# Performance work log

Measured on AMD Instinct MI355X. Metric: run time of the kernel, lower is better.

Reference implementation:

```python
import jax, jax.numpy as jnp
import numpy as np

N = 1_000_000   # total nodes
B = 1024        # number of graphs
H = 64          # node feature dim / LSTM hidden
STEPS = 5       # Set2Set processing steps
PROJ = 128      # projection_dim


def setup_inputs() -> dict:
    key = jax.random.key(0)
    ks = jax.random.split(key, 12)
    x = jax.random.normal(ks[0], (N, H), dtype=jnp.float32)
    batch = jnp.sort(jax.random.randint(ks[1], (N,), 0, B)).astype(jnp.int64)
    s = 1.0 / np.sqrt(H)
    # torch.nn.LSTM(input_size=2H, hidden_size=H), gate order i,f,g,o
    W_ih = jax.random.uniform(ks[2], (4 * H, 2 * H), minval=-s, maxval=s, dtype=jnp.float32)
    W_hh = jax.random.uniform(ks[3], (4 * H, H), minval=-s, maxval=s, dtype=jnp.float32)
    b_ih = jax.random.uniform(ks[4], (4 * H,), minval=-s, maxval=s, dtype=jnp.float32)
    b_hh = jax.random.uniform(ks[5], (4 * H,), minval=-s, maxval=s, dtype=jnp.float32)
    s1 = 1.0 / np.sqrt(2 * H)
    W1 = jax.random.uniform(ks[6], (256, 2 * H), minval=-s1, maxval=s1, dtype=jnp.float32)
    b1 = jax.random.uniform(ks[7], (256,), minval=-s1, maxval=s1, dtype=jnp.float32)
    s2 = 1.0 / np.sqrt(256)
    W2 = jax.random.uniform(ks[8], (PROJ, 256), minval=-s2, maxval=s2, dtype=jnp.float32)
    b2 = jax.random.uniform(ks[9], (PROJ,), minval=-s2, maxval=s2, dtype=jnp.float32)
    return {"x": x, "batch": batch, "W_ih": W_ih, "W_hh": W_hh, "b_ih": b_ih,
            "b_hh": b_hh, "W1": W1, "b1": b1, "W2": W2, "b2": b2}


def _set2set(x, batch, W_ih, W_hh, b_ih, b_hh):
    q_star = jnp.zeros((B, 2 * H), x.dtype)
    h = jnp.zeros((B, H), x.dtype)
    c = jnp.zeros((B, H), x.dtype)
    for _ in range(STEPS):
        gates = q_star @ W_ih.T + b_ih + h @ W_hh.T + b_hh
        i, f, g, o = jnp.split(gates, 4, axis=-1)
        i = jax.nn.sigmoid(i); f = jax.nn.sigmoid(f)
        g = jnp.tanh(g); o = jax.nn.sigmoid(o)
        c = f * c + i * g
        h = o * jnp.tanh(c)
        q = h  # [B, H]
        # segment-wise attention over ragged node sets
        e = jnp.sum(x * q[batch], axis=-1)                         # [N]
        emax = jax.ops.segment_max(e, batch, num_segments=B)       # [B]
        a = jnp.exp(e - emax[batch])
        denom = jax.ops.segment_sum(a, batch, num_segments=B)
        a = a / jnp.maximum(denom, 1e-16)[batch]
        r = jax.ops.segment_sum(a[:, None] * x, batch, num_segments=B)  # [B, H]
        q_star = jnp.concatenate([q, r], axis=-1)
    return q_star


def reference(x, batch, W_ih, W_hh, b_ih, b_hh, W1, b1, W2, b2):
    out = _set2set(x, batch, W_ih, W_hh, b_ih, b_hh)   # [B, 2H]
    out = out @ W1.T + b1                               # [B, 256]
    out = jax.nn.relu(out) @ W2.T + b2                  # [B, PROJ]
    return out
```

## Files before the change

### kernel.cpp

```cpp
#include <hip/hip_runtime.h>
#include <float.h>
#include <math.h>

#define NB 1024
#define HD 64
#define NSTEPS 5
#define SPLIT 4

__device__ __forceinline__ float sigmoidf_(float x) {
    return 1.0f / (1.0f + __expf(-x));
}

__global__ void seg_bounds_kernel(const int* __restrict__ batch,
                                  int* __restrict__ seg_start, int n) {
    int i = blockIdx.x * blockDim.x + threadIdx.x;
    if (i >= n) return;
    int b = batch[i];
    if (i == 0) {
        for (int j = 0; j <= b; ++j) seg_start[j] = 0;
    } else {
        int pb = batch[i - 1];
        for (int j = pb + 1; j <= b; ++j) seg_start[j] = i;
    }
    if (i == n - 1) {
        for (int j = b + 1; j <= NB; ++j) seg_start[j] = n;
    }
}

__global__ void lstm_kernel(const float* __restrict__ W_ih,
                            const float* __restrict__ W_hh,
                            const float* __restrict__ b_ih,
                            const float* __restrict__ b_hh,
                            const float* __restrict__ pm,
                            const float* __restrict__ ps,
                            const float* __restrict__ pr,
                            float* __restrict__ h,
                            float* __restrict__ c,
                            int first) {
    const int G = 8;
    int g0 = blockIdx.x * G;
    __shared__ float s_qs[G][128];
    __shared__ float s_gates[G][256];
    int tid = threadIdx.x;

    if (!first) {
        for (int idx = tid; idx < G * 64; idx += 256) {
            int g = idx >> 6, k = idx & 63;
            s_qs[g][k] = h[(g0 + g) * 64 + k];
        }
        for (int idx = tid; idx < G * 64; idx += 256) {
            int g = idx >> 6, k = idx & 63;
            int b = g0 + g;
            float m0 = pm[b * SPLIT + 0], m1 = pm[b * SPLIT + 1];
            float m2 = pm[b * SPLIT + 2], m3 = pm[b * SPLIT + 3];
            float M = fmaxf(fmaxf(m0, m1), fmaxf(m2, m3));
            float w0 = __expf(m0 - M), w1 = __expf(m1 - M);
            float w2 = __expf(m2 - M), w3 = __expf(m3 - M);
            float S = ps[b * SPLIT + 0] * w0 + ps[b * SPLIT + 1] * w1
                    + ps[b * SPLIT + 2] * w2 + ps[b * SPLIT + 3] * w3;
            float rf = pr[(b * SPLIT + 0) * 64 + k] * w0
                     + pr[(b * SPLIT + 1) * 64 + k] * w1
                     + pr[(b * SPLIT + 2) * 64 + k] * w2
                     + pr[(b * SPLIT + 3) * 64 + k] * w3;
            s_qs[g][64 + k] = rf / fmaxf(S, 1e-16f);
        }
        __syncthreads();
    }

    int j = tid;
    float acc[G];
    float bias = b_ih[j] + b_hh[j];
#pragma unroll
    for (int g = 0; g < G; ++g) acc[g] = bias;

    if (!first) {
        const float4* wih = (const float4*)(W_ih + j * 128);
#pragma unroll 4
        for (int k4 = 0; k4 < 32; ++k4) {
            float4 w = wih[k4];
#pragma unroll
            for (int g = 0; g < G; ++g) {
                acc[g] = fmaf(w.x, s_qs[g][k4 * 4 + 0], acc[g]);
                acc[g] = fmaf(w.y, s_qs[g][k4 * 4 + 1], acc[g]);
                acc[g] = fmaf(w.z, s_qs[g][k4 * 4 + 2], acc[g]);
                acc[g] = fmaf(w.w, s_qs[g][k4 * 4 + 3], acc[g]);
            }
        }
        const float4* whh = (const float4*)(W_hh + j * 64);
#pragma unroll 4
        for (int k4 = 0; k4 < 16; ++k4) {
            float4 w = whh[k4];
#pragma unroll
            for (int g = 0; g < G; ++g) {
                acc[g] = fmaf(w.x, s_qs[g][k4 * 4 + 0], acc[g]);
                acc[g] = fmaf(w.y, s_qs[g][k4 * 4 + 1], acc[g]);
                acc[g] = fmaf(w.z, s_qs[g][k4 * 4 + 2], acc[g]);
                acc[g] = fmaf(w.w, s_qs[g][k4 * 4 + 3], acc[g]);
            }
        }
    }
#pragma unroll
    for (int g = 0; g < G; ++g) s_gates[g][j] = acc[g];
    __syncthreads();

    for (int idx = tid; idx < G * 64; idx += 256) {
        int g = idx >> 6, jj = idx & 63;
        int gb = g0 + g;
        float ig = sigmoidf_(s_gates[g][jj]);
        float fg = sigmoidf_(s_gates[g][jj + 64]);
        float gg = tanhf(s_gates[g][jj + 128]);
        float og = sigmoidf_(s_gates[g][jj + 192]);
        float cprev = first ? 0.0f : c[gb * 64 + jj];
        float cn = fmaf(fg, cprev, ig * gg);
        float hn = og * tanhf(cn);
        c[gb * 64 + jj] = cn;
        h[gb * 64 + jj] = hn;
    }
}

__global__ __launch_bounds__(256) void attn_kernel(const float* __restrict__ x,
                                                   const int* __restrict__ seg_start,
                                                   const float* __restrict__ h,
                                                   float* __restrict__ pm,
                                                   float* __restrict__ ps,
                                                   float* __restrict__ pr) {
    int bs = blockIdx.x;
    int b = bs >> 2;
    int slice = bs & (SPLIT - 1);
    int s0 = seg_start[b], e0 = seg_start[b + 1];
    int len = e0 - s0;
    int s = s0 + (int)(((long long)len * slice) >> 2);
    int e = s0 + (int)(((long long)len * (slice + 1)) >> 2);

    int tid = threadIdx.x;
    int lane = tid & 63;
    int wave = tid >> 6;
    int quad = lane >> 2;
    int p = lane & 3;

    float q[16];
    const float* qsrc = h + b * 64 + p * 16;
#pragma unroll
    for (int k = 0; k < 16; ++k) q[k] = qsrc[k];

    float m = -FLT_MAX, sum = 0.0f;
    float r[16];
#pragma unroll
    for (int k = 0; k < 16; ++k) r[k] = 0.0f;

    for (int base = s; base < e; base += 64) {
        int node = base + wave * 16 + quad;
        bool valid = node < e;
        int nc = valid ? node : (e - 1);
        const float4* xp = (const float4*)(x + (size_t)nc * 64 + p * 16);
        float4 a0 = xp[0], a1 = xp[1], a2 = xp[2], a3 = xp[3];
        float xv[16];
        xv[0] = a0.x; xv[1] = a0.y; xv[2] = a0.z; xv[3] = a0.w;
        xv[4] = a1.x; xv[5] = a1.y; xv[6] = a1.z; xv[7] = a1.w;
        xv[8] = a2.x; xv[9] = a2.y; xv[10] = a2.z; xv[11] = a2.w;
        xv[12] = a3.x; xv[13] = a3.y; xv[14] = a3.z; xv[15] = a3.w;

        float dot = 0.0f;
#pragma unroll
        for (int k = 0; k < 16; ++k) dot = fmaf(xv[k], q[k], dot);
        dot += __shfl_xor(dot, 1);
        dot += __shfl_xor(dot, 2);

        float eeff = valid ? dot : -FLT_MAX;
        float nm = fmaxf(m, eeff);
        float scale = __expf(m - nm);
        float w = valid ? __expf(eeff - nm) : 0.0f;
        sum = fmaf(sum, scale, w);
#pragma unroll
        for (int k = 0; k < 16; ++k) r[k] = fmaf(r[k], scale, w * xv[k]);
        m = nm;
    }

#pragma unroll
    for (int off = 4; off < 64; off <<= 1) {
        float om = __shfl_xor(m, off);
        float os = __shfl_xor(sum, off);
        float orr[16];
#pragma unroll
        for (int k = 0; k < 16; ++k) orr[k] = __shfl_xor(r[k], off);
        float nm = fmaxf(m, om);
        float sc1 = __expf(m - nm);
        float sc2 = __expf(om - nm);
        sum = sum * sc1 + os * sc2;
#pragma unroll
        for (int k = 0; k < 16; ++k) r[k] = r[k] * sc1 + orr[k] * sc2;
        m = nm;
    }

    __shared__ float lm[4], ls[4], lr[4][64];
    if (lane < 4) {
        if (lane == 0) { lm[wave] = m; ls[wave] = sum; }
#pragma unroll
        for (int k = 0; k < 16; ++k) lr[wave][lane * 16 + k] = r[k];
    }
    __syncthreads();
    if (tid < 64) {
        float M = fmaxf(fmaxf(lm[0], lm[1]), fmaxf(lm[2], lm[3]));
        float w0 = __expf(lm[0] - M), w1 = __expf(lm[1] - M);
        float w2 = __expf(lm[2] - M), w3 = __expf(lm[3] - M);
        float S = ls[0] * w0 + ls[1] * w1 + ls[2] * w2 + ls[3] * w3;
        float rf = lr[0][tid] * w0 + lr[1][tid] * w1 + lr[2][tid] * w2 + lr[3][tid] * w3;
        if (tid == 0) { pm[bs] = M; ps[bs] = S; }
        pr[bs * 64 + tid] = rf;
    }
}

__global__ void mlp_kernel(const float* __restrict__ h,
                           const float* __restrict__ pm,
                           const float* __restrict__ ps,
                           const float* __restrict__ pr,
                           const float* __restrict__ W1,
                           const float* __restrict__ b1,
                           const float* __restrict__ W2,
                           const float* __restrict__ b2,
                           float* __restrict__ out) {
    int b = blockIdx.x;
    __shared__ float qs[128];
    __shared__ float hid[256];
    int tid = threadIdx.x;
    if (tid < 64) {
        qs[tid] = h[b * 64 + tid];
    } else if (tid < 128) {
        int k = tid - 64;
        float m0 = pm[b * SPLIT + 0], m1 = pm[b * SPLIT + 1];
        float m2 = pm[b * SPLIT + 2], m3 = pm[b * SPLIT + 3];
        float M = fmaxf(fmaxf(m0, m1), fmaxf(m2, m3));
        float w0 = __expf(m0 - M), w1 = __expf(m1 - M);
        float w2 = __expf(m2 - M), w3 = __expf(m3 - M);
        float S = ps[b * SPLIT + 0] * w0 + ps[b * SPLIT + 1] * w1
                + ps[b * SPLIT + 2] * w2 + ps[b * SPLIT + 3] * w3;
        float rf = pr[(b * SPLIT + 0) * 64 + k] * w0
                 + pr[(b * SPLIT + 1) * 64 + k] * w1
                 + pr[(b * SPLIT + 2) * 64 + k] * w2
                 + pr[(b * SPLIT + 3) * 64 + k] * w3;
        qs[tid] = rf / fmaxf(S, 1e-16f);
    }
    __syncthreads();
    float acc = b1[tid];
    const float4* w = (const float4*)(W1 + tid * 128);
#pragma unroll 4
    for (int k4 = 0; k4 < 32; ++k4) {
        float4 ww = w[k4];
        acc = fmaf(ww.x, qs[k4 * 4 + 0], acc);
        acc = fmaf(ww.y, qs[k4 * 4 + 1], acc);
        acc = fmaf(ww.z, qs[k4 * 4 + 2], acc);
        acc = fmaf(ww.w, qs[k4 * 4 + 3], acc);
    }
    hid[tid] = fmaxf(acc, 0.0f);
    __syncthreads();
    if (tid < 128) {
        float acc2 = b2[tid];
        const float4* w2 = (const float4*)(W2 + tid * 256);
#pragma unroll 4
        for (int k4 = 0; k4 < 64; ++k4) {
            float4 ww = w2[k4];
            acc2 = fmaf(ww.x, hid[k4 * 4 + 0], acc2);
            acc2 = fmaf(ww.y, hid[k4 * 4 + 1], acc2);
            acc2 = fmaf(ww.z, hid[k4 * 4 + 2], acc2);
            acc2 = fmaf(ww.w, hid[k4 * 4 + 3], acc2);
        }
        out[b * 128 + tid] = acc2;
    }
}

extern "C" void kernel_launch(void* const* d_in, const int* in_sizes, int n_in,
                              void* d_out, int out_size, void* d_ws, size_t ws_size,
                              hipStream_t stream) {
    const float* x    = (const float*)d_in[0];
    const int*   batch= (const int*)d_in[1];
    const float* W_ih = (const float*)d_in[2];
    const float* W_hh = (const float*)d_in[3];
    const float* b_ih = (const float*)d_in[4];
    const float* b_hh = (const float*)d_in[5];
    const float* W1   = (const float*)d_in[6];
    const float* b1   = (const float*)d_in[7];
    const float* W2   = (const float*)d_in[8];
    const float* b2   = (const float*)d_in[9];
    float* out = (float*)d_out;
    const int N = in_sizes[1];

    float* h   = (float*)d_ws;
    float* c   = h + NB * 64;
    int*   seg = (int*)(c + NB * 64);
    float* pm  = (float*)(seg + NB + 8);
    float* ps  = pm + NB * SPLIT;
    float* pr  = ps + NB * SPLIT;

    seg_bounds_kernel<<<(N + 255) / 256, 256, 0, stream>>>(batch, seg, N);

    for (int step = 0; step < NSTEPS; ++step) {
        lstm_kernel<<<NB / 8, 256, 0, stream>>>(W_ih, W_hh, b_ih, b_hh,
                                                pm, ps, pr, h, c, step == 0 ? 1 : 0);
        attn_kernel<<<NB * SPLIT, 256, 0, stream>>>(x, seg, h, pm, ps, pr);
    }
    mlp_kernel<<<NB, 256, 0, stream>>>(h, pm, ps, pr, W1, b1, W2, b2, out);
}
```

Before: 618.9 us.

## Remap attention lanes so each wave loads contiguous float4 rows per node

The attention kernel's thread-to-data mapping changes. Each node's 64 features are now split across 16 lanes with one float4 each, instead of 4 lanes with 16 floats each. A wave's loads now cover fully contiguous 1 KB chunks, and each thread holds far fewer registers for q and r. The cost is more shuffle steps in the dot-product reduction and an online-softmax update per sub-step, which adds more exp calls per node.

```diff
diff --git a/kernel.cpp b/kernel.cpp
--- a/kernel.cpp
+++ b/kernel.cpp
@@ -135,68 +135,69 @@
     int tid = threadIdx.x;
     int lane = tid & 63;
     int wave = tid >> 6;
-    int quad = lane >> 2;
-    int p = lane & 3;
-
-    float q[16];
-    const float* qsrc = h + b * 64 + p * 16;
-#pragma unroll
-    for (int k = 0; k < 16; ++k) q[k] = qsrc[k];
+    int fc = lane & 15;
+    int grp = lane >> 4;
+
+    float4 q4 = *(const float4*)(h + b * 64 + fc * 4);
 
     float m = -FLT_MAX, sum = 0.0f;
-    float r[16];
-#pragma unroll
-    for (int k = 0; k < 16; ++k) r[k] = 0.0f;
-
-    for (int base = s; base < e; base += 64) {
-        int node = base + wave * 16 + quad;
-        bool valid = node < e;
-        int nc = valid ? node : (e - 1);
-        const float4* xp = (const float4*)(x + (size_t)nc * 64 + p * 16);
-        float4 a0 = xp[0], a1 = xp[1], a2 = xp[2], a3 = xp[3];
-        float xv[16];
-        xv[0] = a0.x; xv[1] = a0.y; xv[2] = a0.z; xv[3] = a0.w;
-        xv[4] = a1.x; xv[5] = a1.y; xv[6] = a1.z; xv[7] = a1.w;
-        xv[8] = a2.x; xv[9] = a2.y; xv[10] = a2.z; xv[11] = a2.w;
-        xv[12] = a3.x; xv[13] = a3.y; xv[14] = a3.z; xv[15] = a3.w;
-
-        float dot = 0.0f;
-#pragma unroll
-        for (int k = 0; k < 16; ++k) dot = fmaf(xv[k], q[k], dot);
-        dot += __shfl_xor(dot, 1);
-        dot += __shfl_xor(dot, 2);
-
-        float eeff = valid ? dot : -FLT_MAX;
-        float nm = fmaxf(m, eeff);
-        float scale = __expf(m - nm);
-        float w = valid ? __expf(eeff - nm) : 0.0f;
-        sum = fmaf(sum, scale, w);
-#pragma unroll
-        for (int k = 0; k < 16; ++k) r[k] = fmaf(r[k], scale, w * xv[k]);
-        m = nm;
-    }
-
-#pragma unroll
-    for (int off = 4; off < 64; off <<= 1) {
+    float4 r4 = make_float4(0.0f, 0.0f, 0.0f, 0.0f);
+
+    const int maxidx4 = e * 16 - 1;
+    for (int base = s + wave * 16; base < e; base += 64) {
+#pragma unroll
+        for (int t = 0; t < 4; ++t) {
+            int node = base + t * 4 + grp;
+            int idx4 = base * 16 + t * 64 + lane;
+            idx4 = min(idx4, maxidx4);
+            float4 xv = *(const float4*)(x + (size_t)idx4 * 4);
+
+            float d = xv.x * q4.x;
+            d = fmaf(xv.y, q4.y, d);
+            d = fmaf(xv.z, q4.z, d);
+            d = fmaf(xv.w, q4.w, d);
+            d += __shfl_xor(d, 1);
+            d += __shfl_xor(d, 2);
+            d += __shfl_xor(d, 4);
+            d += __shfl_xor(d, 8);
+
+            bool valid = node < e;
+            float eeff = valid ? d : -FLT_MAX;
+            float nm = fmaxf(m, eeff);
+            float sc = __expf(m - nm);
+            float w = valid ? __expf(eeff - nm) : 0.0f;
+            sum = fmaf(sum, sc, w);
+            r4.x = fmaf(r4.x, sc, w * xv.x);
+            r4.y = fmaf(r4.y, sc, w * xv.y);
+            r4.z = fmaf(r4.z, sc, w * xv.z);
+            r4.w = fmaf(r4.w, sc, w * xv.w);
+            m = nm;
+        }
+    }
+
+#pragma unroll
+    for (int off = 16; off < 64; off <<= 1) {
         float om = __shfl_xor(m, off);
         float os = __shfl_xor(sum, off);
-        float orr[16];
-#pragma unroll
-        for (int k = 0; k < 16; ++k) orr[k] = __shfl_xor(r[k], off);
+        float ox = __shfl_xor(r4.x, off);
+        float oy = __shfl_xor(r4.y, off);
+        float oz = __shfl_xor(r4.z, off);
+        float ow = __shfl_xor(r4.w, off);
         float nm = fmaxf(m, om);
-        float sc1 = __expf(m - nm);
-        float sc2 = __expf(om - nm);
-        sum = sum * sc1 + os * sc2;
-#pragma unroll
-        for (int k = 0; k < 16; ++k) r[k] = r[k] * sc1 + orr[k] * sc2;
+        float s1 = __expf(m - nm);
+        float s2 = __expf(om - nm);
+        sum = sum * s1 + os * s2;
+        r4.x = r4.x * s1 + ox * s2;
+        r4.y = r4.y * s1 + oy * s2;
+        r4.z = r4.z * s1 + oz * s2;
+        r4.w = r4.w * s1 + ow * s2;
         m = nm;
     }
 
     __shared__ float lm[4], ls[4], lr[4][64];
-    if (lane < 4) {
+    if (lane < 16) {
         if (lane == 0) { lm[wave] = m; ls[wave] = sum; }
-#pragma unroll
-        for (int k = 0; k < 16; ++k) lr[wave][lane * 16 + k] = r[k];
+        *(float4*)&lr[wave][lane * 4] = r4;
     }
     __syncthreads();
     if (tid < 64) {
```

New measurement: 614.6 us. About the same (-0.7%).
